# Kernel tuning notes

Measured on AMD Instinct MI355X. Metric: run time of the kernel, lower is better.

The kernel has to match this reference:

```python
import jax, jax.numpy as jnp
import numpy as np

NUM_HEADS = 16


def rotate_half(x):
    h = x.shape[-1] // 2
    return jnp.concatenate([-x[..., h:], x[..., :h]], axis=-1)


def setup_inputs() -> dict:
    key = jax.random.key(0)
    ks = jax.random.split(key, 8)
    S, dim, hd = 8192, 1280, 80
    n_seg = 8
    hidden_states = jax.random.normal(ks[0], (S, dim), dtype=jnp.float32)
    cu_seqlens = (jnp.arange(n_seg + 1, dtype=jnp.int32) * (S // n_seg))
    ang = jax.random.uniform(ks[1], (S, hd), dtype=jnp.float32) * (2.0 * np.pi)
    cos = jnp.cos(ang)
    sin = jnp.sin(ang)
    qkv_w = jax.random.normal(ks[2], (3 * dim, dim), dtype=jnp.float32) * (dim ** -0.5)
    qkv_b = jax.random.normal(ks[3], (3 * dim,), dtype=jnp.float32) * 0.02
    proj_w = jax.random.normal(ks[4], (dim, dim), dtype=jnp.float32) * (dim ** -0.5)
    proj_b = jax.random.normal(ks[5], (dim,), dtype=jnp.float32) * 0.02
    return {"hidden_states": hidden_states, "cu_seqlens": cu_seqlens,
            "cos": cos, "sin": sin, "qkv_w": qkv_w, "qkv_b": qkv_b,
            "proj_w": proj_w, "proj_b": proj_b}


def reference(hidden_states, cu_seqlens, cos, sin, qkv_w, qkv_b, proj_w, proj_b):
    S, dim = hidden_states.shape
    H = NUM_HEADS
    hd = dim // H
    scaling = hd ** -0.5

    # qkv projection: [S, 3*dim] -> [S, 3, H, hd]
    qkv = (hidden_states @ qkv_w.T + qkv_b).reshape(S, 3, H, hd)
    q, k, v = qkv[:, 0], qkv[:, 1], qkv[:, 2]  # each [S, H, hd]

    # RoPE in float32, cos/sin broadcast over heads
    c = cos[:, None, :].astype(jnp.float32)
    s = sin[:, None, :].astype(jnp.float32)
    qf, kf = q.astype(jnp.float32), k.astype(jnp.float32)
    q = (qf * c + rotate_half(qf) * s).astype(q.dtype)
    k = (kf * c + rotate_half(kf) * s).astype(k.dtype)

    # Block-diagonal varlen attention: equal-length segments -> batch dim
    lengths = np.diff(np.asarray(cu_seqlens))
    L = int(lengths[0])
    assert (lengths == L).all(), "reference assumes uniform segment lengths"
    B = lengths.shape[0]
    qb = q.reshape(B, L, H, hd)
    kb = k.reshape(B, L, H, hd)
    vb = v.reshape(B, L, H, hd)

    scores = jnp.einsum('blhd,bmhd->bhlm', qb, kb) * scaling
    probs = jax.nn.softmax(scores.astype(jnp.float32), axis=-1).astype(scores.dtype)
    out = jnp.einsum('bhlm,bmhd->blhd', probs, vb).reshape(S, dim)

    return out @ proj_w.T + proj_b
```

## Files before the change

### kernel.cpp

```cpp
#include <hip/hip_runtime.h>
#include <math.h>

typedef _Float16 f16;
typedef _Float16 half8 __attribute__((ext_vector_type(8)));
typedef _Float16 half4v __attribute__((ext_vector_type(4)));
typedef _Float16 half2v __attribute__((ext_vector_type(2)));
typedef float floatx4 __attribute__((ext_vector_type(4)));
typedef unsigned int u32;

#define AS1 __attribute__((address_space(1)))
#define AS3 __attribute__((address_space(3)))

__device__ __forceinline__ void stage16(f16* l, const f16* g) {
    __builtin_amdgcn_global_load_lds((const AS1 u32*)g, (AS3 u32*)l, 16, 0, 0);
}

__global__ __launch_bounds__(256) void cvt_f32_f16(const float* __restrict__ in,
                                                   f16* __restrict__ out, int n4) {
    int i = blockIdx.x * blockDim.x + threadIdx.x;
    if (i >= n4) return;
    float4 v = ((const float4*)in)[i];
    half4v h = {(f16)v.x, (f16)v.y, (f16)v.z, (f16)v.w};
    ((half4v*)out)[i] = h;
}

__global__ __launch_bounds__(256) void pack_w(const float* __restrict__ Wf,
                                              f16* __restrict__ Wp) {
    const int p = blockIdx.x * 256 + threadIdx.x;
    const int lane = p & 63;
    const int j = (p >> 6) & 3;
    const int sk = p >> 8;
    const int k0 = sk % 40;
    const int slab = sk / 40;
    const int row = slab * 64 + j * 16 + (lane & 15);
    const int col = k0 * 32 + (lane >> 4) * 8;
    const float* src = Wf + (size_t)row * 1280 + col;
    float4 a = *(const float4*)src;
    float4 b = *(const float4*)(src + 4);
    half8 h = {(f16)a.x, (f16)a.y, (f16)a.z, (f16)a.w,
               (f16)b.x, (f16)b.y, (f16)b.z, (f16)b.w};
    *(half8*)(Wp + (size_t)p * 8) = h;
}

constexpr int GK = 1280;

__global__ __launch_bounds__(256) void gemm_nt(const f16* __restrict__ A,
                                               const f16* __restrict__ Bp,
                                               const float* __restrict__ bias,
                                               f16* __restrict__ outH,
                                               float* __restrict__ outF, int N) {
    __shared__ f16 As[128 * 32];
    const int t = threadIdx.x;
    const int lane = t & 63;
    const int w = t >> 6;
    const int wm = w & 1, wn = w >> 1;
    const int c16 = lane & 15, quad = lane >> 4;
    const size_t bm = blockIdx.x, bn = blockIdx.y;
    const f16* Ab = A + bm * 128 * GK;
    const f16* Bw = Bp + (size_t)(bn * 2 + wn) * (40 * 4 * 64 * 8);
    floatx4 acc[4][4] = {};
    const int c0 = t, c1 = t + 256;
    const int r0 = c0 >> 2, kc0 = ((c0 & 3) - (r0 >> 1)) & 3;
    const int r1 = c1 >> 2, kc1 = ((c1 & 3) - (r1 >> 1)) & 3;
    for (int k0i = 0; k0i < 40; k0i++) {
        const int k0 = k0i * 32;
        stage16(As + c0 * 8, Ab + (size_t)r0 * GK + k0 + kc0 * 8);
        stage16(As + c1 * 8, Ab + (size_t)r1 * GK + k0 + kc1 * 8);
        half8 bf[4];
#pragma unroll
        for (int j = 0; j < 4; j++)
            bf[j] = *(const half8*)(Bw + (((size_t)k0i * 4 + j) * 64 + lane) * 8);
        __syncthreads();
        half8 af[4];
#pragma unroll
        for (int i = 0; i < 4; i++) {
            const int row = wm * 64 + i * 16 + c16;
            af[i] = *(const half8*)(As + (4 * row + ((quad + (row >> 1)) & 3)) * 8);
        }
#pragma unroll
        for (int i = 0; i < 4; i++)
#pragma unroll
            for (int j = 0; j < 4; j++)
                acc[i][j] = __builtin_amdgcn_mfma_f32_16x16x32_f16(af[i], bf[j], acc[i][j], 0, 0, 0);
        __syncthreads();
    }
#pragma unroll
    for (int i = 0; i < 4; i++) {
#pragma unroll
        for (int j = 0; j < 4; j++) {
            const int col = (int)bn * 128 + wn * 64 + j * 16 + c16;
            const float bv = bias[col];
#pragma unroll
            for (int r = 0; r < 4; r++) {
                const size_t row = bm * 128 + wm * 64 + i * 16 + quad * 4 + r;
                const float v = acc[i][j][r] + bv;
                if (outH) outH[row * (size_t)N + col] = (f16)v;
                else      outF[row * (size_t)N + col] = v;
            }
        }
    }
}

#define QSCALE (0.11180339887498949f * 1.4426950408889634f)

__global__ __launch_bounds__(320) void rope_kernel(const f16* __restrict__ qkv,
                                                   const float* __restrict__ cosp,
                                                   const float* __restrict__ sinp,
                                                   f16* __restrict__ qb, f16* __restrict__ kb,
                                                   f16* __restrict__ vt) {
    constexpr int S = 8192;
    const int bs = blockIdx.x, h = blockIdx.y, t = threadIdx.x;
    const int sl = t / 5, g = t % 5;
    const int s = bs * 64 + sl;
    {
        const size_t base = (size_t)s * 3840 + h * 80 + g * 8;
        half8 qa = *(const half8*)(qkv + base);
        half8 qc = *(const half8*)(qkv + base + 40);
        half8 ka = *(const half8*)(qkv + base + 1280);
        half8 kc = *(const half8*)(qkv + base + 1320);
        const float* cp = cosp + (size_t)s * 80 + g * 8;
        const float* sp = sinp + (size_t)s * 80 + g * 8;
        half8 qo0, qo1, ko0, ko1;
#pragma unroll
        for (int j = 0; j < 8; j++) {
            float c0 = cp[j], c1 = cp[j + 40];
            float n0 = sp[j], n1 = sp[j + 40];
            float q0 = (float)qa[j], q1 = (float)qc[j];
            float k0 = (float)ka[j], k1 = (float)kc[j];
            qo0[j] = (f16)((q0 * c0 - q1 * n0) * QSCALE);
            qo1[j] = (f16)((q1 * c1 + q0 * n1) * QSCALE);
            ko0[j] = (f16)(k0 * c0 - k1 * n0);
            ko1[j] = (f16)(k1 * c1 + k0 * n1);
        }
        const size_t ob = ((size_t)h * S + s) * 96 + g * 8;
        *(half8*)(qb + ob)      = qo0;
        *(half8*)(qb + ob + 40) = qo1;
        *(half8*)(kb + ob)      = ko0;
        *(half8*)(kb + ob + 40) = ko1;
        if (g < 2) {
            half8 qp = {}, kp = {};
            if (g == 0) { qp[0] = (f16)(-8.0f); kp[0] = (f16)(1.0f); }
            const size_t pb = ((size_t)h * S + s) * 96 + 80 + g * 8;
            *(half8*)(qb + pb) = qp;
            *(half8*)(kb + pb) = kp;
        }
    }
    __shared__ f16 vls[64][81];
    for (int j = t; j < 64 * 80; j += 320) {
        int s2 = j / 80, d = j % 80;
        vls[s2][d] = qkv[((size_t)(bs * 64 + s2)) * 3840 + 2560 + h * 80 + d];
    }
    __syncthreads();
    for (int j = t; j < 64 * 80; j += 320) {
        int d = j >> 6, s2 = j & 63;
        vt[((size_t)(h * 80 + d)) * S + bs * 64 + s2] = vls[s2][d];
    }
}

__global__ __launch_bounds__(256, 2) void attn_kernel(const f16* __restrict__ qb,
                                                      const f16* __restrict__ kb,
                                                      const f16* __restrict__ vt,
                                                      const int* __restrict__ cu,
                                                      f16* __restrict__ out) {
    constexpr int S = 8192;
    __shared__ f16 Ks[2][64 * 96];
    __shared__ f16 Ps[256 * 72];
    const int t = threadIdx.x, lane = t & 63, w = t >> 6;
    const int c16 = lane & 15, quad = lane >> 4;
    const int id = blockIdx.x;
    const int pair = id & 127;
    const int qt = id >> 7;
    const int h = pair & 15, z = pair >> 4;
    const int s0 = cu[z];

    half8 qf[4][3];
#pragma unroll
    for (int qt2 = 0; qt2 < 4; qt2++)
#pragma unroll
        for (int ks = 0; ks < 3; ks++)
            qf[qt2][ks] = *(const half8*)(qb + ((size_t)h * S + s0 + qt * 256 + w * 64 + qt2 * 16 + c16) * 96 + ks * 32 + quad * 8);

    const f16 ov = (c16 == 0) ? (f16)1.f : (f16)0.f;
    const half8 onesf = {ov, ov, ov, ov, ov, ov, ov, ov};

    const int sR = t >> 2;
    const int sK = ((t & 3) - (sR >> 1)) & 3;

    {
        const f16* Kg = kb + ((size_t)h * S + s0) * 96;
#pragma unroll
        for (int j = 0; j < 3; j++)
            stage16(&Ks[0][0] + (j * 256 + t) * 8, Kg + (size_t)sR * 96 + j * 32 + sK * 8);
    }
    __syncthreads();

    floatx4 o[6][4] = {};

    for (int kv = 0; kv < 16; kv++) {
        if (kv < 15) {
            const f16* Kg = kb + ((size_t)h * S + s0 + (kv + 1) * 64) * 96;
            f16* Kd = &Ks[(kv + 1) & 1][0];
#pragma unroll
            for (int j = 0; j < 3; j++)
                stage16(Kd + (j * 256 + t) * 8, Kg + (size_t)sR * 96 + j * 32 + sK * 8);
        }
        const f16* Kc = &Ks[kv & 1][0];
        floatx4 sc[4][4] = {};
#pragma unroll
        for (int ks = 0; ks < 3; ks++) {
            half8 kf[4];
#pragma unroll
            for (int mt = 0; mt < 4; mt++) {
                const int row = mt * 16 + c16;
                kf[mt] = *(const half8*)(Kc + (ks * 256 + 4 * row + ((quad + (row >> 1)) & 3)) * 8);
            }
#pragma unroll
            for (int qt2 = 0; qt2 < 4; qt2++)
#pragma unroll
                for (int mt = 0; mt < 4; mt++)
                    sc[mt][qt2] = __builtin_amdgcn_mfma_f32_16x16x32_f16(kf[mt], qf[qt2][ks], sc[mt][qt2], 0, 0, 0);
        }
#pragma unroll
        for (int qt2 = 0; qt2 < 4; qt2++) {
            const int q = w * 64 + qt2 * 16 + c16;
#pragma unroll
            for (int mt = 0; mt < 4; mt++) {
                half4v pv;
#pragma unroll
                for (int r = 0; r < 4; r++)
                    pv[r] = (f16)__builtin_amdgcn_exp2f(sc[mt][qt2][r]);
                *(half4v*)(Ps + q * 72 + mt * 16 + quad * 4) = pv;
            }
        }
#pragma unroll
        for (int ks = 0; ks < 2; ks++) {
            const f16* Vg = vt + (size_t)h * 80 * S + s0 + kv * 64 + ks * 32;
            half8 vf[5];
#pragma unroll
            for (int dt = 0; dt < 5; dt++)
                vf[dt] = *(const half8*)(Vg + (size_t)(dt * 16 + c16) * S + quad * 8);
#pragma unroll
            for (int qt2 = 0; qt2 < 4; qt2++) {
                const int q = w * 64 + qt2 * 16 + c16;
                half8 pf = *(const half8*)(Ps + q * 72 + ks * 32 + quad * 8);
#pragma unroll
                for (int dt = 0; dt < 5; dt++)
                    o[dt][qt2] = __builtin_amdgcn_mfma_f32_16x16x32_f16(vf[dt], pf, o[dt][qt2], 0, 0, 0);
                o[5][qt2] = __builtin_amdgcn_mfma_f32_16x16x32_f16(onesf, pf, o[5][qt2], 0, 0, 0);
            }
        }
        __syncthreads();
    }
#pragma unroll
    for (int qt2 = 0; qt2 < 4; qt2++) {
        const float l = __shfl(o[5][qt2][0], c16);
        const float inv = 1.f / l;
        const size_t srow = (size_t)s0 + qt * 256 + w * 64 + qt2 * 16 + c16;
#pragma unroll
        for (int dt = 0; dt < 5; dt++)
#pragma unroll
            for (int rp = 0; rp < 2; rp++) {
                half2v hv = {(f16)(o[dt][qt2][rp * 2] * inv), (f16)(o[dt][qt2][rp * 2 + 1] * inv)};
                *(half2v*)(out + srow * 1280 + h * 80 + dt * 16 + quad * 4 + rp * 2) = hv;
            }
    }
}

extern "C" void kernel_launch(void* const* d_in, const int* in_sizes, int n_in,
                              void* d_out, int out_size, void* d_ws, size_t ws_size,
                              hipStream_t stream) {
    const float* hidden = (const float*)d_in[0];
    const int* cu       = (const int*)d_in[1];
    const float* cosp   = (const float*)d_in[2];
    const float* sinp   = (const float*)d_in[3];
    const float* qkv_w  = (const float*)d_in[4];
    const float* qkv_b  = (const float*)d_in[5];
    const float* proj_w = (const float*)d_in[6];
    const float* proj_b = (const float*)d_in[7];
    float* out = (float*)d_out;

    constexpr size_t S = 8192, DIM = 1280, N3 = 3840;
    f16* A16   = (f16*)d_ws;
    f16* WP16  = A16 + S * DIM;
    f16* PP16  = WP16 + N3 * DIM;
    f16* QKV16 = PP16 + DIM * DIM;
    f16* QB    = QKV16 + S * N3;
    f16* KB    = QB + (size_t)16 * S * 96;
    f16* VT    = KB + (size_t)16 * S * 96;
    f16* AT16  = A16;

    {
        int n4 = (int)(S * DIM / 4);
        cvt_f32_f16<<<(n4 + 255) / 256, 256, 0, stream>>>(hidden, A16, n4);
    }
    pack_w<<<(int)(N3 * DIM / 8 / 256), 256, 0, stream>>>(qkv_w, WP16);
    pack_w<<<(int)(DIM * DIM / 8 / 256), 256, 0, stream>>>(proj_w, PP16);
    gemm_nt<<<dim3(64, 30), 256, 0, stream>>>(A16, WP16, qkv_b, QKV16, nullptr, 3840);
    rope_kernel<<<dim3(128, 16), 320, 0, stream>>>(QKV16, cosp, sinp, QB, KB, VT);
    attn_kernel<<<512, 256, 0, stream>>>(QB, KB, VT, cu, AT16);
    gemm_nt<<<dim3(64, 10), 256, 0, stream>>>(AT16, PP16, proj_b, nullptr, out, 1280);
}
```

Measured before the change: 360.3 us.

## Replace GEMM with 256x256 LDS-staged double-buffered kernel and plain weight conversion

Replaces the 128x128 GEMM, which read pre-packed weights directly from global memory, with a 512-thread 256x256-tile kernel. The new kernel stages both A and B into double-buffered LDS using async global-to-LDS loads, interleaved with four MFMA clusters per 64-wide K step. It adds s_setprio hints and an XCD-aware block remapping. Weight packing is replaced by a plain f32-to-f16 conversion, since B now goes through the swizzled LDS path. The proj GEMM launches only 160 blocks, which may underfill the GPU, and the many barriers add synchronisation cost.

```diff
diff --git a/kernel.cpp b/kernel.cpp
--- a/kernel.cpp
+++ b/kernel.cpp
@@ -13,6 +13,12 @@
 
 __device__ __forceinline__ void stage16(f16* l, const f16* g) {
     __builtin_amdgcn_global_load_lds((const AS1 u32*)g, (AS3 u32*)l, 16, 0, 0);
+}
+
+__device__ __forceinline__ void barrier_mem() {
+    asm volatile("" ::: "memory");
+    __builtin_amdgcn_s_barrier();
+    asm volatile("" ::: "memory");
 }
 
 __global__ __launch_bounds__(256) void cvt_f32_f16(const float* __restrict__ in,
@@ -24,78 +30,123 @@
     ((half4v*)out)[i] = h;
 }
 
-__global__ __launch_bounds__(256) void pack_w(const float* __restrict__ Wf,
-                                              f16* __restrict__ Wp) {
-    const int p = blockIdx.x * 256 + threadIdx.x;
-    const int lane = p & 63;
-    const int j = (p >> 6) & 3;
-    const int sk = p >> 8;
-    const int k0 = sk % 40;
-    const int slab = sk / 40;
-    const int row = slab * 64 + j * 16 + (lane & 15);
-    const int col = k0 * 32 + (lane >> 4) * 8;
-    const float* src = Wf + (size_t)row * 1280 + col;
-    float4 a = *(const float4*)src;
-    float4 b = *(const float4*)(src + 4);
-    half8 h = {(f16)a.x, (f16)a.y, (f16)a.z, (f16)a.w,
-               (f16)b.x, (f16)b.y, (f16)b.z, (f16)b.w};
-    *(half8*)(Wp + (size_t)p * 8) = h;
-}
-
 constexpr int GK = 1280;
-
-__global__ __launch_bounds__(256) void gemm_nt(const f16* __restrict__ A,
-                                               const f16* __restrict__ Bp,
-                                               const float* __restrict__ bias,
-                                               f16* __restrict__ outH,
-                                               float* __restrict__ outF, int N) {
-    __shared__ f16 As[128 * 32];
+constexpr int KT = 20;
+
+__device__ __forceinline__ void stage_q(const f16* __restrict__ g, f16* l, int t) {
+#pragma unroll
+    for (int u = 0; u < 2; u++) {
+        const int c = t + u * 512;
+        const int row = c >> 2;
+        const int lc = ((c & 3) - (row >> 1)) & 3;
+        stage16(l + c * 8, g + (size_t)row * GK + lc * 8);
+    }
+}
+
+#define MMA_CLUSTER(AF, BF, MB)                                               \
+    asm volatile("s_waitcnt lgkmcnt(0)" ::: "memory");                        \
+    __builtin_amdgcn_s_setprio(1);                                            \
+    _Pragma("unroll")                                                         \
+    for (int m_ = 0; m_ < 4; m_++) {                                          \
+        _Pragma("unroll")                                                     \
+        for (int n_ = 0; n_ < 4; n_++)                                        \
+            acc[MB + m_][n_] = __builtin_amdgcn_mfma_f32_16x16x32_f16(        \
+                AF[m_], BF[n_], acc[MB + m_][n_], 0, 0, 0);                   \
+    }                                                                         \
+    __builtin_amdgcn_s_setprio(0);
+
+__global__ __launch_bounds__(512, 2) void gemm256(const f16* __restrict__ A,
+                                                  const f16* __restrict__ B,
+                                                  const float* __restrict__ bias,
+                                                  f16* __restrict__ outH,
+                                                  float* __restrict__ outF,
+                                                  int N, int NT) {
+    __shared__ f16 sm[2][4][8192];
     const int t = threadIdx.x;
-    const int lane = t & 63;
-    const int w = t >> 6;
-    const int wm = w & 1, wn = w >> 1;
+    const int lane = t & 63, w = t >> 6;
+    const int wm = w >> 2, wn = w & 3;
     const int c16 = lane & 15, quad = lane >> 4;
-    const size_t bm = blockIdx.x, bn = blockIdx.y;
-    const f16* Ab = A + bm * 128 * GK;
-    const f16* Bw = Bp + (size_t)(bn * 2 + wn) * (40 * 4 * 64 * 8);
-    floatx4 acc[4][4] = {};
-    const int c0 = t, c1 = t + 256;
-    const int r0 = c0 >> 2, kc0 = ((c0 & 3) - (r0 >> 1)) & 3;
-    const int r1 = c1 >> 2, kc1 = ((c1 & 3) - (r1 >> 1)) & 3;
-    for (int k0i = 0; k0i < 40; k0i++) {
-        const int k0 = k0i * 32;
-        stage16(As + c0 * 8, Ab + (size_t)r0 * GK + k0 + kc0 * 8);
-        stage16(As + c1 * 8, Ab + (size_t)r1 * GK + k0 + kc1 * 8);
-        half8 bf[4];
-#pragma unroll
-        for (int j = 0; j < 4; j++)
-            bf[j] = *(const half8*)(Bw + (((size_t)k0i * 4 + j) * 64 + lane) * 8);
-        __syncthreads();
-        half8 af[4];
-#pragma unroll
-        for (int i = 0; i < 4; i++) {
-            const int row = wm * 64 + i * 16 + c16;
-            af[i] = *(const half8*)(As + (4 * row + ((quad + (row >> 1)) & 3)) * 8);
-        }
-#pragma unroll
-        for (int i = 0; i < 4; i++)
-#pragma unroll
-            for (int j = 0; j < 4; j++)
-                acc[i][j] = __builtin_amdgcn_mfma_f32_16x16x32_f16(af[i], bf[j], acc[i][j], 0, 0, 0);
-        __syncthreads();
-    }
-#pragma unroll
-    for (int i = 0; i < 4; i++) {
-#pragma unroll
-        for (int j = 0; j < 4; j++) {
-            const int col = (int)bn * 128 + wn * 64 + j * 16 + c16;
-            const float bv = bias[col];
+    const int id = blockIdx.x;
+    const int nx = (int)gridDim.x >> 3;
+    const int gid = (id & 7) * nx + (id >> 3);
+    const int bm = gid / NT, bn = gid % NT;
+    const f16* Ab = A + (size_t)bm * 256 * GK;
+    const f16* Bb = B + (size_t)bn * 256 * GK;
+
+    floatx4 acc[8][4] = {};
+
+    auto rdA = [&](const f16* q, int mh, half8(&af)[4]) {
+#pragma unroll
+        for (int m = 0; m < 4; m++) {
+            const int r = wm * 128 + mh * 64 + m * 16 + c16;
+            af[m] = *(const half8*)(q + r * 32 + (((quad + (r >> 1)) & 3) * 8));
+        }
+    };
+    auto rdB = [&](const f16* q, half8(&bf)[4]) {
+#pragma unroll
+        for (int n = 0; n < 4; n++) {
+            const int r = wn * 64 + n * 16 + c16;
+            bf[n] = *(const half8*)(q + r * 32 + (((quad + (r >> 1)) & 3) * 8));
+        }
+    };
+
+    stage_q(Bb + 0,  &sm[0][2][0], t); asm volatile("" ::: "memory");
+    stage_q(Ab + 0,  &sm[0][0][0], t); asm volatile("" ::: "memory");
+    stage_q(Bb + 32, &sm[0][3][0], t); asm volatile("" ::: "memory");
+    stage_q(Ab + 32, &sm[0][1][0], t); asm volatile("" ::: "memory");
+    stage_q(Bb + 64, &sm[1][2][0], t); asm volatile("" ::: "memory");
+    stage_q(Ab + 64, &sm[1][0][0], t); asm volatile("" ::: "memory");
+    stage_q(Bb + 96, &sm[1][3][0], t); asm volatile("" ::: "memory");
+
+    for (int kt = 0; kt < KT; kt++) {
+        const int p = kt & 1;
+        const f16* qA0 = &sm[p][0][0];
+        const f16* qA1 = &sm[p][1][0];
+        const f16* qB0 = &sm[p][2][0];
+        const f16* qB1 = &sm[p][3][0];
+        if (kt == KT - 1) { asm volatile("s_waitcnt vmcnt(0)" ::: "memory"); }
+        else              { asm volatile("s_waitcnt vmcnt(6)" ::: "memory"); }
+        barrier_mem();
+
+        half8 af[4], bf0[4], bf1[4];
+        rdB(qB0, bf0);
+        rdA(qA0, 0, af);
+        if (kt + 1 < KT) stage_q(Ab + (size_t)(kt + 1) * 64 + 32, &sm[p ^ 1][1][0], t);
+        barrier_mem();
+        MMA_CLUSTER(af, bf0, 0);
+        barrier_mem();
+        rdA(qA0, 1, af);
+        if (kt + 2 < KT) stage_q(Bb + (size_t)(kt + 2) * 64, &sm[p][2][0], t);
+        barrier_mem();
+        MMA_CLUSTER(af, bf0, 4);
+        barrier_mem();
+        rdB(qB1, bf1);
+        rdA(qA1, 0, af);
+        if (kt + 2 < KT) stage_q(Ab + (size_t)(kt + 2) * 64, &sm[p][0][0], t);
+        barrier_mem();
+        MMA_CLUSTER(af, bf1, 0);
+        barrier_mem();
+        rdA(qA1, 1, af);
+        if (kt + 2 < KT) stage_q(Bb + (size_t)(kt + 2) * 64 + 32, &sm[p][3][0], t);
+        barrier_mem();
+        MMA_CLUSTER(af, bf1, 4);
+        barrier_mem();
+    }
+
+    const int colBase = bn * 256 + wn * 64;
+    const size_t rowBase = (size_t)bm * 256 + wm * 128;
+#pragma unroll
+    for (int n = 0; n < 4; n++) {
+        const int col = colBase + n * 16 + c16;
+        const float bv = bias[col];
+#pragma unroll
+        for (int m = 0; m < 8; m++) {
+            const size_t row = rowBase + m * 16 + quad * 4;
 #pragma unroll
             for (int r = 0; r < 4; r++) {
-                const size_t row = bm * 128 + wm * 64 + i * 16 + quad * 4 + r;
-                const float v = acc[i][j][r] + bv;
-                if (outH) outH[row * (size_t)N + col] = (f16)v;
-                else      outF[row * (size_t)N + col] = v;
+                const float v = acc[m][n][r] + bv;
+                if (outH) outH[(row + r) * (size_t)N + col] = (f16)v;
+                else      outF[(row + r) * (size_t)N + col] = v;
             }
         }
     }
@@ -281,9 +332,9 @@
 
     constexpr size_t S = 8192, DIM = 1280, N3 = 3840;
     f16* A16   = (f16*)d_ws;
-    f16* WP16  = A16 + S * DIM;
-    f16* PP16  = WP16 + N3 * DIM;
-    f16* QKV16 = PP16 + DIM * DIM;
+    f16* W16   = A16 + S * DIM;
+    f16* P16   = W16 + N3 * DIM;
+    f16* QKV16 = P16 + DIM * DIM;
     f16* QB    = QKV16 + S * N3;
     f16* KB    = QB + (size_t)16 * S * 96;
     f16* VT    = KB + (size_t)16 * S * 96;
@@ -293,10 +344,16 @@
         int n4 = (int)(S * DIM / 4);
         cvt_f32_f16<<<(n4 + 255) / 256, 256, 0, stream>>>(hidden, A16, n4);
     }
-    pack_w<<<(int)(N3 * DIM / 8 / 256), 256, 0, stream>>>(qkv_w, WP16);
-    pack_w<<<(int)(DIM * DIM / 8 / 256), 256, 0, stream>>>(proj_w, PP16);
-    gemm_nt<<<dim3(64, 30), 256, 0, stream>>>(A16, WP16, qkv_b, QKV16, nullptr, 3840);
+    {
+        int n4 = (int)(N3 * DIM / 4);
+        cvt_f32_f16<<<(n4 + 255) / 256, 256, 0, stream>>>(qkv_w, W16, n4);
+    }
+    {
+        int n4 = (int)(DIM * DIM / 4);
+        cvt_f32_f16<<<(n4 + 255) / 256, 256, 0, stream>>>(proj_w, P16, n4);
+    }
+    gemm256<<<32 * 15, 512, 0, stream>>>(A16, W16, qkv_b, QKV16, nullptr, 3840, 15);
     rope_kernel<<<dim3(128, 16), 320, 0, stream>>>(QKV16, cosp, sinp, QB, KB, VT);
-    attn_kernel<<<512, 256, 0, stream>>>(QB, KB, VT, cu, AT16);
-    gemm_nt<<<dim3(64, 10), 256, 0, stream>>>(AT16, PP16, proj_b, nullptr, out, 1280);
-}
+    attn_kernel<<<512, 256, 0, stream>>>(QB, KB, VT, cu, A16);
+    gemm256<<<32 * 5, 512, 0, stream>>>(AT16, P16, proj_b, nullptr, out, 1280, 5);
+}
```

Result: slower. 373.6 us (+3.7%).

## Replace GEMM with double-buffered, larger-tile, grid-swizzled pipelined kernel

Applied to the files above, without the earlier changes.

Replaces the single-buffered 128x128 GEMM with a templated kernel that uses 512 threads, 256-column tiles (256 or 128 rows), double-buffered LDS staging and register double-buffering of B fragments. Explicit vmcnt/lgkmcnt waits and raw barriers let the next k-tile's loads overlap the current MFMA work. Block IDs are swizzled in groups of eight to improve L2 reuse. The cost is higher register and LDS pressure, and the hand-tuned wait counts make correctness depend on the exact number of loads issued.

```diff
diff --git a/kernel.cpp b/kernel.cpp
--- a/kernel.cpp
+++ b/kernel.cpp
@@ -43,57 +43,114 @@
 }
 
 constexpr int GK = 1280;
-
-__global__ __launch_bounds__(256) void gemm_nt(const f16* __restrict__ A,
-                                               const f16* __restrict__ Bp,
-                                               const float* __restrict__ bias,
-                                               f16* __restrict__ outH,
-                                               float* __restrict__ outF, int N) {
-    __shared__ f16 As[128 * 32];
+constexpr int KT = 20;
+
+template <int MT>
+__global__ __launch_bounds__(512, 2) void gemm_bp(const f16* __restrict__ A,
+                                                  const f16* __restrict__ Bp,
+                                                  const float* __restrict__ bias,
+                                                  f16* __restrict__ outH,
+                                                  float* __restrict__ outF,
+                                                  int N, int NT) {
+    constexpr int M_FR = MT / 32;
+    constexpr int QE = MT * 32;
+    __shared__ f16 sm[2][2][QE];
     const int t = threadIdx.x;
-    const int lane = t & 63;
-    const int w = t >> 6;
-    const int wm = w & 1, wn = w >> 1;
+    const int lane = t & 63, w = t >> 6;
+    const int wm = w >> 2, wn = w & 3;
     const int c16 = lane & 15, quad = lane >> 4;
-    const size_t bm = blockIdx.x, bn = blockIdx.y;
-    const f16* Ab = A + bm * 128 * GK;
-    const f16* Bw = Bp + (size_t)(bn * 2 + wn) * (40 * 4 * 64 * 8);
-    floatx4 acc[4][4] = {};
-    const int c0 = t, c1 = t + 256;
-    const int r0 = c0 >> 2, kc0 = ((c0 & 3) - (r0 >> 1)) & 3;
-    const int r1 = c1 >> 2, kc1 = ((c1 & 3) - (r1 >> 1)) & 3;
-    for (int k0i = 0; k0i < 40; k0i++) {
-        const int k0 = k0i * 32;
-        stage16(As + c0 * 8, Ab + (size_t)r0 * GK + k0 + kc0 * 8);
-        stage16(As + c1 * 8, Ab + (size_t)r1 * GK + k0 + kc1 * 8);
-        half8 bf[4];
-#pragma unroll
-        for (int j = 0; j < 4; j++)
-            bf[j] = *(const half8*)(Bw + (((size_t)k0i * 4 + j) * 64 + lane) * 8);
-        __syncthreads();
-        half8 af[4];
-#pragma unroll
-        for (int i = 0; i < 4; i++) {
-            const int row = wm * 64 + i * 16 + c16;
-            af[i] = *(const half8*)(As + (4 * row + ((quad + (row >> 1)) & 3)) * 8);
-        }
-#pragma unroll
-        for (int i = 0; i < 4; i++)
+    const int id = blockIdx.x;
+    const int nx = (int)gridDim.x >> 3;
+    const int gid = (id & 7) * nx + (id >> 3);
+    const int bm = gid / NT, bn = gid - bm * NT;
+    const f16* Ab = A + (size_t)bm * MT * GK;
+    const f16* Bw = Bp + (size_t)(bn * 4 + wn) * (40 * 4 * 64 * 8) + lane * 8;
+
+    floatx4 acc[M_FR][4] = {};
+    half8 bfA[8], bfB[8];
+
+    auto stageA = [&](int kt, int dst) {
+#pragma unroll
+        for (int ks = 0; ks < 2; ks++)
+#pragma unroll
+            for (int u = 0; u < MT / 128; u++) {
+                const int c = t + u * 512;
+                const int row = c >> 2;
+                const int lc = ((c & 3) - (row >> 1)) & 3;
+                stage16(&sm[dst][ks][0] + c * 8,
+                        Ab + (size_t)row * GK + kt * 64 + ks * 32 + lc * 8);
+            }
+    };
+    auto loadB = [&](int kt, half8(&bf)[8]) {
+#pragma unroll
+        for (int ks = 0; ks < 2; ks++)
 #pragma unroll
             for (int j = 0; j < 4; j++)
-                acc[i][j] = __builtin_amdgcn_mfma_f32_16x16x32_f16(af[i], bf[j], acc[i][j], 0, 0, 0);
-        __syncthreads();
-    }
-#pragma unroll
-    for (int i = 0; i < 4; i++) {
-#pragma unroll
-        for (int j = 0; j < 4; j++) {
-            const int col = (int)bn * 128 + wn * 64 + j * 16 + c16;
-            const float bv = bias[col];
-#pragma unroll
-            for (int r = 0; r < 4; r++) {
-                const size_t row = bm * 128 + wm * 64 + i * 16 + quad * 4 + r;
-                const float v = acc[i][j][r] + bv;
+                bf[ks * 4 + j] = *(const half8*)(Bw + (size_t)((kt * 2 + ks) * 4 + j) * 512);
+    };
+    auto compute = [&](int p, half8(&bf)[8]) {
+#pragma unroll
+        for (int ks = 0; ks < 2; ks++) {
+            const f16* q = &sm[p][ks][0];
+#pragma unroll
+            for (int m = 0; m < M_FR; m++) {
+                const int r = wm * (MT / 2) + m * 16 + c16;
+                half8 a = *(const half8*)(q + r * 32 + (((quad + (r >> 1)) & 3) * 8));
+#pragma unroll
+                for (int n = 0; n < 4; n++)
+                    acc[m][n] = __builtin_amdgcn_mfma_f32_16x16x32_f16(a, bf[ks * 4 + n],
+                                                                       acc[m][n], 0, 0, 0);
+            }
+        }
+    };
+#define WAIT_STEADY()                                              \
+    if constexpr (MT == 256) {                                     \
+        asm volatile("s_waitcnt vmcnt(12)" ::: "memory");          \
+    } else {                                                       \
+        asm volatile("s_waitcnt vmcnt(10)" ::: "memory");          \
+    }
+
+    stageA(0, 0);
+    loadB(0, bfA);
+    asm volatile("s_waitcnt vmcnt(8)" ::: "memory");
+    __builtin_amdgcn_s_barrier();
+
+    for (int i = 0; i < 10; i++) {
+        const int k0 = 2 * i;
+        asm volatile("s_waitcnt lgkmcnt(0)" ::: "memory");
+        __builtin_amdgcn_s_barrier();
+        stageA(k0 + 1, 1);
+        loadB(k0 + 1, bfB);
+        WAIT_STEADY();
+        __builtin_amdgcn_s_barrier();
+        compute(0, bfA);
+        asm volatile("s_waitcnt lgkmcnt(0)" ::: "memory");
+        __builtin_amdgcn_s_barrier();
+        if (i < 9) {
+            stageA(k0 + 2, 0);
+            loadB(k0 + 2, bfA);
+            WAIT_STEADY();
+        } else {
+            asm volatile("s_waitcnt vmcnt(0)" ::: "memory");
+        }
+        __builtin_amdgcn_s_barrier();
+        compute(1, bfB);
+    }
+
+    const int colBase = bn * 256 + wn * 64;
+    const size_t rowBase = (size_t)bm * MT + wm * (MT / 2);
+    float bv[4];
+#pragma unroll
+    for (int n = 0; n < 4; n++) bv[n] = bias[colBase + n * 16 + c16];
+#pragma unroll
+    for (int m = 0; m < M_FR; m++) {
+#pragma unroll
+        for (int r = 0; r < 4; r++) {
+            const size_t row = rowBase + m * 16 + quad * 4 + r;
+#pragma unroll
+            for (int n = 0; n < 4; n++) {
+                const int col = colBase + n * 16 + c16;
+                const float v = acc[m][n][r] + bv[n];
                 if (outH) outH[row * (size_t)N + col] = (f16)v;
                 else      outF[row * (size_t)N + col] = v;
             }
@@ -295,8 +352,8 @@
     }
     pack_w<<<(int)(N3 * DIM / 8 / 256), 256, 0, stream>>>(qkv_w, WP16);
     pack_w<<<(int)(DIM * DIM / 8 / 256), 256, 0, stream>>>(proj_w, PP16);
-    gemm_nt<<<dim3(64, 30), 256, 0, stream>>>(A16, WP16, qkv_b, QKV16, nullptr, 3840);
+    gemm_bp<256><<<32 * 15, 512, 0, stream>>>(A16, WP16, qkv_b, QKV16, nullptr, 3840, 15);
     rope_kernel<<<dim3(128, 16), 320, 0, stream>>>(QKV16, cosp, sinp, QB, KB, VT);
-    attn_kernel<<<512, 256, 0, stream>>>(QB, KB, VT, cu, AT16);
-    gemm_nt<<<dim3(64, 10), 256, 0, stream>>>(AT16, PP16, proj_b, nullptr, out, 1280);
-}
+    attn_kernel<<<512, 256, 0, stream>>>(QB, KB, VT, cu, A16);
+    gemm_bp<128><<<64 * 5, 512, 0, stream>>>(AT16, PP16, proj_b, nullptr, out, 1280, 5);
+}
```

Result: slower. 375.8 us (+4.3%).
